# Optimization experiments

Hardware: AMD Instinct MI355X
Metric: run time of the kernel (lower is better)

Reference implementation:

```python
import jax, jax.numpy as jnp
import numpy as np

S = 7          # side
B = 2          # boxes per cell
C = 20         # classes
L = S * S      # grid cells
NOOBJ = 0.5 * 1.0
OBJ   = 0.5 * 1.0
CLS   = 0.5 * 1.0
COORD = 0.5 * 5.0


def setup_inputs() -> dict:
    key = jax.random.key(0)
    k1, k2, k3 = jax.random.split(key, 3)
    n = 16384
    preds = jax.random.uniform(k1, (n, L * (C + 5 * B)), dtype=jnp.float32)
    labels = jax.random.uniform(k2, (n, L * (1 + C + 4)), dtype=jnp.float32)
    lab = labels.reshape(n, L, 1 + C + 4)
    obj_flag = (jax.random.uniform(k3, (n, L)) < 0.15).astype(jnp.float32)
    lab = lab.at[:, :, 0].set(obj_flag)
    labels = lab.reshape(n, -1)
    return {"preds": preds, "labels": labels}


def _iou(t, o):
    # t, o: [..., 4] boxes in (cx, cy, w, h); returns [...]
    left   = jnp.maximum(t[..., 0] - 0.5 * t[..., 2], o[..., 0] - 0.5 * o[..., 2])
    right  = jnp.minimum(t[..., 0] + 0.5 * t[..., 2], o[..., 0] + 0.5 * o[..., 2])
    top    = jnp.maximum(t[..., 1] - 0.5 * t[..., 3], o[..., 1] - 0.5 * o[..., 3])
    bottom = jnp.minimum(t[..., 1] + 0.5 * t[..., 3], o[..., 1] + 0.5 * o[..., 3])
    w = right - left
    h = bottom - top
    invalid = (w < 0) | (h < 0)
    inter = jnp.where(invalid, 0.0, w * h)
    union = t[..., 2] * t[..., 3] + o[..., 2] * o[..., 3] - inter
    return jnp.where(invalid, 0.0, inter / jnp.maximum(union, 1e-12))


def reference(preds, labels):
    n = preds.shape[0]
    pcls  = preds[:, : L * C].reshape(n, L, C)                       # [n,L,C]
    pconf = preds[:, L * C : L * C + L * B].reshape(n, L, B)          # [n,L,B]
    pbox  = preds[:, L * C + L * B :].reshape(n, L, B, 4)             # [n,L,B,4]

    lab  = labels.reshape(n, L, 1 + C + 4)
    obj  = lab[:, :, 0] != 0                                          # [n,L]
    tcls = lab[:, :, 1 : 1 + C]                                       # [n,L,C]
    tbox = lab[:, :, 1 + C :]                                         # [n,L,4] raw

    # --- best-box selection (on detached predictions, like .detach() in torch) ---
    o_raw = jax.lax.stop_gradient(pbox)
    o = jnp.concatenate([o_raw[..., :2] / S, o_raw[..., 2:] ** 2], axis=-1)      # [n,L,B,4]
    t = jnp.concatenate([tbox[..., :2] / S, tbox[..., 2:]], axis=-1)[:, :, None] # [n,L,1,4]
    t = jax.lax.stop_gradient(t)

    iou  = _iou(t, o)                                                 # [n,L,B]
    rmse = jnp.sqrt(jnp.sum((t - o) ** 2, axis=-1))                   # [n,L,B]
    max_iou = jnp.max(iou, axis=-1)
    # if any IoU>0 pick first argmax of IoU, else first argmin of RMSE (best_rmse init 20)
    best = jnp.where(max_iou > 0, jnp.argmax(iou, axis=-1), jnp.argmin(rmse, axis=-1))  # [n,L]
    best_iou = jnp.take_along_axis(iou, best[:, :, None], axis=-1)[..., 0]        # [n,L]

    onehot = jnp.arange(B) == best[:, :, None]                        # [n,L,B]
    mask_best = obj[:, :, None] & onehot

    # confidence delta: noobject everywhere, overwritten at best box of object cells
    conf_delta = jnp.where(mask_best,
                           OBJ * (best_iou[:, :, None] - pconf) ** 2,
                           NOOBJ * pconf ** 2)

    # class delta (object cells only)
    cls_delta = jnp.where(obj[:, :, None], CLS * (tcls - pcls) ** 2, 0.0)

    # coord delta at best box: raw truth x,y and sqrt(truth w,h) vs raw preds
    pbest = jnp.take_along_axis(pbox, best[:, :, None, None], axis=2)[:, :, 0]    # [n,L,4]
    ttarget = jnp.concatenate([tbox[..., :2], jnp.sqrt(tbox[..., 2:])], axis=-1)  # [n,L,4]
    coord_delta = jnp.where(obj[:, :, None], COORD * (ttarget - pbest) ** 2, 0.0)

    return jnp.nansum(conf_delta) + jnp.nansum(cls_delta) + jnp.nansum(coord_delta)
```

## Files before the change

kernel.cpp:

```cpp
#include <hip/hip_runtime.h>


#define L_CELLS 49
#define PRED_ROW 1470
#define LAB_ROW 1225
#define CONF_BASE 980
#define BOX_BASE 1078
#define W_NOOBJ 0.5f
#define W_OBJ 0.5f
#define W_CLS 0.5f
#define W_COORD 2.5f
#define INV_S (1.0f / 7.0f)

__global__ __launch_bounds__(256) void yolo_loss_kernel(
    const float* __restrict__ preds, const float* __restrict__ labels,
    float* __restrict__ ws, int n) {
  int cell = blockIdx.x * blockDim.x + threadIdx.x;
  int total = n * L_CELLS;
  float acc = 0.0f;
  if (cell < total) {
    int sample = cell / L_CELLS;
    int l = cell - sample * L_CELLS;
    const float* rp = preds + (size_t)sample * PRED_ROW;
    const float* labc = labels + (size_t)sample * LAB_ROW + l * 25;

    float objf = labc[0];
    const float2 cf = *(const float2*)(rp + CONF_BASE + 2 * l);
    float c0 = cf.x, c1 = cf.y;

    if (objf != 0.0f) {
      const float* boxp = rp + BOX_BASE + 8 * l;
      float bx[8];
#pragma unroll
      for (int k = 0; k < 4; ++k) {
        float2 v = *(const float2*)(boxp + 2 * k);
        bx[2 * k] = v.x;
        bx[2 * k + 1] = v.y;
      }

      float tx = labc[21], ty = labc[22], tw = labc[23], th = labc[24];
      float t0 = tx * INV_S, t1 = ty * INV_S, t2 = tw, t3 = th;

      float iou[2], rmse2[2];
#pragma unroll
      for (int b = 0; b < 2; ++b) {
        float o0 = bx[4 * b + 0] * INV_S;
        float o1 = bx[4 * b + 1] * INV_S;
        float o2 = bx[4 * b + 2] * bx[4 * b + 2];
        float o3 = bx[4 * b + 3] * bx[4 * b + 3];
        float left = fmaxf(t0 - 0.5f * t2, o0 - 0.5f * o2);
        float right = fminf(t0 + 0.5f * t2, o0 + 0.5f * o2);
        float top = fmaxf(t1 - 0.5f * t3, o1 - 0.5f * o3);
        float bot = fminf(t1 + 0.5f * t3, o1 + 0.5f * o3);
        float w = right - left;
        float h = bot - top;
        bool invalid = (w < 0.0f) || (h < 0.0f);
        float inter = invalid ? 0.0f : w * h;
        float uni = t2 * t3 + o2 * o3 - inter;
        iou[b] = invalid ? 0.0f : inter / fmaxf(uni, 1e-12f);
        float d0 = t0 - o0, d1 = t1 - o1, d2 = t2 - o2, d3 = t3 - o3;
        rmse2[b] = d0 * d0 + d1 * d1 + d2 * d2 + d3 * d3;
      }

      float max_iou = fmaxf(iou[0], iou[1]);
      int best;
      if (max_iou > 0.0f)
        best = (iou[1] > iou[0]) ? 1 : 0;
      else
        best = (rmse2[1] < rmse2[0]) ? 1 : 0;
      float best_iou = iou[best];

      float cb = (best == 0) ? c0 : c1;
      float co = (best == 0) ? c1 : c0;
      float db = best_iou - cb;
      acc += W_OBJ * db * db + W_NOOBJ * co * co;

      const float* pcls = rp + l * 20;
      float clsacc = 0.0f;
#pragma unroll
      for (int c = 0; c < 20; ++c) {
        float d = labc[1 + c] - pcls[c];
        clsacc += d * d;
      }
      acc += W_CLS * clsacc;

      float e0 = tx - bx[best * 4 + 0];
      float e1 = ty - bx[best * 4 + 1];
      float e2 = sqrtf(tw) - bx[best * 4 + 2];
      float e3 = sqrtf(th) - bx[best * 4 + 3];
      acc += W_COORD * (e0 * e0 + e1 * e1 + e2 * e2 + e3 * e3);
    } else {
      acc = W_NOOBJ * (c0 * c0 + c1 * c1);
    }
  }

#pragma unroll
  for (int off = 32; off > 0; off >>= 1) acc += __shfl_down(acc, off);

  __shared__ float wsum[4];
  int wave = threadIdx.x >> 6;
  int lane = threadIdx.x & 63;
  if (lane == 0) wsum[wave] = acc;
  __syncthreads();
  if (threadIdx.x == 0) {
    ws[blockIdx.x] = wsum[0] + wsum[1] + wsum[2] + wsum[3];
  }
}

__global__ __launch_bounds__(256) void final_reduce_kernel(
    const float* __restrict__ ws, float* __restrict__ out, int m) {
  float acc = 0.0f;
  for (int i = threadIdx.x; i < m; i += 256) acc += ws[i];
#pragma unroll
  for (int off = 32; off > 0; off >>= 1) acc += __shfl_down(acc, off);
  __shared__ float wsum[4];
  int wave = threadIdx.x >> 6;
  int lane = threadIdx.x & 63;
  if (lane == 0) wsum[wave] = acc;
  __syncthreads();
  if (threadIdx.x == 0) out[0] = wsum[0] + wsum[1] + wsum[2] + wsum[3];
}

extern "C" void kernel_launch(void* const* d_in, const int* in_sizes, int n_in,
                              void* d_out, int out_size, void* d_ws, size_t ws_size,
                              hipStream_t stream) {
  const float* preds = (const float*)d_in[0];
  const float* labels = (const float*)d_in[1];
  float* out = (float*)d_out;
  float* ws = (float*)d_ws;
  int n = in_sizes[0] / PRED_ROW;
  int total = n * L_CELLS;
  int blocks = (total + 255) / 256;

  yolo_loss_kernel<<<blocks, 256, 0, stream>>>(preds, labels, ws, n);
  final_reduce_kernel<<<1, 256, 0, stream>>>(ws, out, blocks);
}
```

Baseline: 189.1 us.

## Stage per-sample rows in LDS with coalesced float4 loads, block per two samples

Each block now handles two samples. It copies their full prediction and label rows into shared memory with aligned float4 loads, then computes the class loss spread across all threads, one (cell, class) element each, while 49 threads handle the box and confidence logic. This replaces strided, uncoalesced per-cell global reads with contiguous vector loads. In exchange it reads every row in full even though only about 15% of cells need class data, and it adds LDS traffic, a block barrier and many idle threads during the box phase. The block count assumes n is divisible by two.

```diff
diff --git a/kernel.cpp b/kernel.cpp
--- a/kernel.cpp
+++ b/kernel.cpp
@@ -11,86 +11,113 @@
 #define W_CLS 0.5f
 #define W_COORD 2.5f
 #define INV_S (1.0f / 7.0f)
+#define SPB 2
 
 __global__ __launch_bounds__(256) void yolo_loss_kernel(
     const float* __restrict__ preds, const float* __restrict__ labels,
     float* __restrict__ ws, int n) {
-  int cell = blockIdx.x * blockDim.x + threadIdx.x;
-  int total = n * L_CELLS;
+  __shared__ float4 lab4[SPB][308];
+  __shared__ float4 pred4[SPB][368];
+
+  const int tid = threadIdx.x;
+  const int s0 = blockIdx.x * SPB;
+
+  const size_t ltotal = (size_t)n * LAB_ROW;
+  const size_t ptotal = (size_t)n * PRED_ROW;
+
+  int loff[SPB], poff[SPB];
+#pragma unroll
+  for (int r = 0; r < SPB; ++r) {
+    size_t lrow = (size_t)(s0 + r) * LAB_ROW;
+    size_t lstart = lrow & ~(size_t)3;
+    loff[r] = (int)(lrow - lstart);
+    for (int i = tid; i < 308; i += 256) {
+      size_t g = lstart + 4 * (size_t)i;
+      if (g > ltotal - 4) g = ltotal - 4;
+      lab4[r][i] = *(const float4*)(labels + g);
+    }
+    size_t prow = (size_t)(s0 + r) * PRED_ROW;
+    size_t pstart = prow & ~(size_t)3;
+    poff[r] = (int)(prow - pstart);
+    for (int i = tid; i < 368; i += 256) {
+      size_t g = pstart + 4 * (size_t)i;
+      if (g > ptotal - 4) g = ptotal - 4;
+      pred4[r][i] = *(const float4*)(preds + g);
+    }
+  }
+  __syncthreads();
+
   float acc = 0.0f;
-  if (cell < total) {
-    int sample = cell / L_CELLS;
-    int l = cell - sample * L_CELLS;
-    const float* rp = preds + (size_t)sample * PRED_ROW;
-    const float* labc = labels + (size_t)sample * LAB_ROW + l * 25;
 
-    float objf = labc[0];
-    const float2 cf = *(const float2*)(rp + CONF_BASE + 2 * l);
-    float c0 = cf.x, c1 = cf.y;
+#pragma unroll
+  for (int r = 0; r < SPB; ++r) {
+    const float* lab = (const float*)lab4[r] + loff[r];
+    const float* pr = (const float*)pred4[r] + poff[r];
 
-    if (objf != 0.0f) {
-      const float* boxp = rp + BOX_BASE + 8 * l;
-      float bx[8];
+    for (int idx = tid; idx < CONF_BASE; idx += 256) {
+      int l = idx / 20;
+      int c = idx - l * 20;
+      if (lab[l * 25] != 0.0f) {
+        float d = lab[l * 25 + 1 + c] - pr[idx];
+        acc += W_CLS * d * d;
+      }
+    }
+
+    if (tid < L_CELLS) {
+      int l = tid;
+      float objf = lab[l * 25];
+      float c0 = pr[CONF_BASE + 2 * l];
+      float c1 = pr[CONF_BASE + 2 * l + 1];
+      if (objf != 0.0f) {
+        float bx[8];
 #pragma unroll
-      for (int k = 0; k < 4; ++k) {
-        float2 v = *(const float2*)(boxp + 2 * k);
-        bx[2 * k] = v.x;
-        bx[2 * k + 1] = v.y;
+        for (int k = 0; k < 8; ++k) bx[k] = pr[BOX_BASE + 8 * l + k];
+        float tx = lab[l * 25 + 21], ty = lab[l * 25 + 22];
+        float tw = lab[l * 25 + 23], th = lab[l * 25 + 24];
+        float t0 = tx * INV_S, t1 = ty * INV_S, t2 = tw, t3 = th;
+
+        float iou[2], rmse2[2];
+#pragma unroll
+        for (int b = 0; b < 2; ++b) {
+          float o0 = bx[4 * b + 0] * INV_S;
+          float o1 = bx[4 * b + 1] * INV_S;
+          float o2 = bx[4 * b + 2] * bx[4 * b + 2];
+          float o3 = bx[4 * b + 3] * bx[4 * b + 3];
+          float left = fmaxf(t0 - 0.5f * t2, o0 - 0.5f * o2);
+          float right = fminf(t0 + 0.5f * t2, o0 + 0.5f * o2);
+          float top = fmaxf(t1 - 0.5f * t3, o1 - 0.5f * o3);
+          float bot = fminf(t1 + 0.5f * t3, o1 + 0.5f * o3);
+          float w = right - left;
+          float h = bot - top;
+          bool invalid = (w < 0.0f) || (h < 0.0f);
+          float inter = invalid ? 0.0f : w * h;
+          float uni = t2 * t3 + o2 * o3 - inter;
+          iou[b] = invalid ? 0.0f : inter / fmaxf(uni, 1e-12f);
+          float d0 = t0 - o0, d1 = t1 - o1, d2 = t2 - o2, d3 = t3 - o3;
+          rmse2[b] = d0 * d0 + d1 * d1 + d2 * d2 + d3 * d3;
+        }
+
+        float max_iou = fmaxf(iou[0], iou[1]);
+        int best;
+        if (max_iou > 0.0f)
+          best = (iou[1] > iou[0]) ? 1 : 0;
+        else
+          best = (rmse2[1] < rmse2[0]) ? 1 : 0;
+        float best_iou = iou[best];
+
+        float cb = (best == 0) ? c0 : c1;
+        float co = (best == 0) ? c1 : c0;
+        float db = best_iou - cb;
+        acc += W_OBJ * db * db + W_NOOBJ * co * co;
+
+        float e0 = tx - bx[best * 4 + 0];
+        float e1 = ty - bx[best * 4 + 1];
+        float e2 = sqrtf(tw) - bx[best * 4 + 2];
+        float e3 = sqrtf(th) - bx[best * 4 + 3];
+        acc += W_COORD * (e0 * e0 + e1 * e1 + e2 * e2 + e3 * e3);
+      } else {
+        acc += W_NOOBJ * (c0 * c0 + c1 * c1);
       }
-
-      float tx = labc[21], ty = labc[22], tw = labc[23], th = labc[24];
-      float t0 = tx * INV_S, t1 = ty * INV_S, t2 = tw, t3 = th;
-
-      float iou[2], rmse2[2];
-#pragma unroll
-      for (int b = 0; b < 2; ++b) {
-        float o0 = bx[4 * b + 0] * INV_S;
-        float o1 = bx[4 * b + 1] * INV_S;
-        float o2 = bx[4 * b + 2] * bx[4 * b + 2];
-        float o3 = bx[4 * b + 3] * bx[4 * b + 3];
-        float left = fmaxf(t0 - 0.5f * t2, o0 - 0.5f * o2);
-        float right = fminf(t0 + 0.5f * t2, o0 + 0.5f * o2);
-        float top = fmaxf(t1 - 0.5f * t3, o1 - 0.5f * o3);
-        float bot = fminf(t1 + 0.5f * t3, o1 + 0.5f * o3);
-        float w = right - left;
-        float h = bot - top;
-        bool invalid = (w < 0.0f) || (h < 0.0f);
-        float inter = invalid ? 0.0f : w * h;
-        float uni = t2 * t3 + o2 * o3 - inter;
-        iou[b] = invalid ? 0.0f : inter / fmaxf(uni, 1e-12f);
-        float d0 = t0 - o0, d1 = t1 - o1, d2 = t2 - o2, d3 = t3 - o3;
-        rmse2[b] = d0 * d0 + d1 * d1 + d2 * d2 + d3 * d3;
-      }
-
-      float max_iou = fmaxf(iou[0], iou[1]);
-      int best;
-      if (max_iou > 0.0f)
-        best = (iou[1] > iou[0]) ? 1 : 0;
-      else
-        best = (rmse2[1] < rmse2[0]) ? 1 : 0;
-      float best_iou = iou[best];
-
-      float cb = (best == 0) ? c0 : c1;
-      float co = (best == 0) ? c1 : c0;
-      float db = best_iou - cb;
-      acc += W_OBJ * db * db + W_NOOBJ * co * co;
-
-      const float* pcls = rp + l * 20;
-      float clsacc = 0.0f;
-#pragma unroll
-      for (int c = 0; c < 20; ++c) {
-        float d = labc[1 + c] - pcls[c];
-        clsacc += d * d;
-      }
-      acc += W_CLS * clsacc;
-
-      float e0 = tx - bx[best * 4 + 0];
-      float e1 = ty - bx[best * 4 + 1];
-      float e2 = sqrtf(tw) - bx[best * 4 + 2];
-      float e3 = sqrtf(th) - bx[best * 4 + 3];
-      acc += W_COORD * (e0 * e0 + e1 * e1 + e2 * e2 + e3 * e3);
-    } else {
-      acc = W_NOOBJ * (c0 * c0 + c1 * c1);
     }
   }
 
@@ -98,13 +125,11 @@
   for (int off = 32; off > 0; off >>= 1) acc += __shfl_down(acc, off);
 
   __shared__ float wsum[4];
-  int wave = threadIdx.x >> 6;
-  int lane = threadIdx.x & 63;
+  int wave = tid >> 6;
+  int lane = tid & 63;
   if (lane == 0) wsum[wave] = acc;
   __syncthreads();
-  if (threadIdx.x == 0) {
-    ws[blockIdx.x] = wsum[0] + wsum[1] + wsum[2] + wsum[3];
-  }
+  if (tid == 0) ws[blockIdx.x] = wsum[0] + wsum[1] + wsum[2] + wsum[3];
 }
 
 __global__ __launch_bounds__(256) void final_reduce_kernel(
@@ -129,8 +154,7 @@
   float* out = (float*)d_out;
   float* ws = (float*)d_ws;
   int n = in_sizes[0] / PRED_ROW;
-  int total = n * L_CELLS;
-  int blocks = (total + 255) / 256;
+  int blocks = n / SPB;
 
   yolo_loss_kernel<<<blocks, 256, 0, stream>>>(preds, labels, ws, n);
   final_reduce_kernel<<<1, 256, 0, stream>>>(ws, out, blocks);
```

Result: slower. 211.3 us (+11.8%).

## Map one wavefront per sample and stage label rows in LDS via float4 loads

Applied to the files above, without the earlier changes.

Each block now handles four samples, one per 64-lane wavefront, with lanes 0-48 mapping to grid cells. The whole label row is first copied into shared memory with coalesced float4 loads, replacing the strided 25-float-per-thread global reads. Class predictions are read as float2. The goal is to cut uncoalesced label traffic. In exchange 15 of 64 lanes sit idle, the kernel assumes n is a multiple of 4, and no barrier separates the LDS writes from the reads, which only works because each wave reads just its own slot.

```diff
diff --git a/kernel.cpp b/kernel.cpp
--- a/kernel.cpp
+++ b/kernel.cpp
@@ -14,31 +14,41 @@
 
 __global__ __launch_bounds__(256) void yolo_loss_kernel(
     const float* __restrict__ preds, const float* __restrict__ labels,
-    float* __restrict__ ws, int n) {
-  int cell = blockIdx.x * blockDim.x + threadIdx.x;
-  int total = n * L_CELLS;
+    float* __restrict__ ws) {
+  __shared__ float4 labs4[4][312];
+
+  const int tid = threadIdx.x;
+  const int w = tid >> 6;
+  const int lane = tid & 63;
+  const int s = blockIdx.x * 4 + w;
+
+  size_t g0 = (size_t)s * LAB_ROW;
+  size_t a = g0 & ~(size_t)3;
+  int off = (int)(g0 - a);
+  for (int i = lane; i < 307; i += 64) {
+    labs4[w][i] = *(const float4*)(labels + a + 4 * (size_t)i);
+  }
+
+  const float* lab = (const float*)labs4[w] + off;
+  const float* rp = preds + (size_t)s * PRED_ROW;
+
   float acc = 0.0f;
-  if (cell < total) {
-    int sample = cell / L_CELLS;
-    int l = cell - sample * L_CELLS;
-    const float* rp = preds + (size_t)sample * PRED_ROW;
-    const float* labc = labels + (size_t)sample * LAB_ROW + l * 25;
-
-    float objf = labc[0];
-    const float2 cf = *(const float2*)(rp + CONF_BASE + 2 * l);
+  if (lane < L_CELLS) {
+    const int l = lane;
+    float2 cf = *(const float2*)(rp + CONF_BASE + 2 * l);
     float c0 = cf.x, c1 = cf.y;
+    float objf = lab[25 * l];
 
     if (objf != 0.0f) {
-      const float* boxp = rp + BOX_BASE + 8 * l;
       float bx[8];
 #pragma unroll
       for (int k = 0; k < 4; ++k) {
-        float2 v = *(const float2*)(boxp + 2 * k);
+        float2 v = *(const float2*)(rp + BOX_BASE + 8 * l + 2 * k);
         bx[2 * k] = v.x;
         bx[2 * k + 1] = v.y;
       }
-
-      float tx = labc[21], ty = labc[22], tw = labc[23], th = labc[24];
+      float tx = lab[25 * l + 21], ty = lab[25 * l + 22];
+      float tw = lab[25 * l + 23], th = lab[25 * l + 24];
       float t0 = tx * INV_S, t1 = ty * INV_S, t2 = tw, t3 = th;
 
       float iou[2], rmse2[2];
@@ -52,10 +62,10 @@
         float right = fminf(t0 + 0.5f * t2, o0 + 0.5f * o2);
         float top = fmaxf(t1 - 0.5f * t3, o1 - 0.5f * o3);
         float bot = fminf(t1 + 0.5f * t3, o1 + 0.5f * o3);
-        float w = right - left;
+        float wd = right - left;
         float h = bot - top;
-        bool invalid = (w < 0.0f) || (h < 0.0f);
-        float inter = invalid ? 0.0f : w * h;
+        bool invalid = (wd < 0.0f) || (h < 0.0f);
+        float inter = invalid ? 0.0f : wd * h;
         float uni = t2 * t3 + o2 * o3 - inter;
         iou[b] = invalid ? 0.0f : inter / fmaxf(uni, 1e-12f);
         float d0 = t0 - o0, d1 = t1 - o1, d2 = t2 - o2, d3 = t3 - o3;
@@ -75,12 +85,13 @@
       float db = best_iou - cb;
       acc += W_OBJ * db * db + W_NOOBJ * co * co;
 
-      const float* pcls = rp + l * 20;
       float clsacc = 0.0f;
 #pragma unroll
-      for (int c = 0; c < 20; ++c) {
-        float d = labc[1 + c] - pcls[c];
-        clsacc += d * d;
+      for (int k = 0; k < 10; ++k) {
+        float2 p = *(const float2*)(rp + 20 * l + 2 * k);
+        float d0 = lab[25 * l + 1 + 2 * k] - p.x;
+        float d1 = lab[25 * l + 2 + 2 * k] - p.y;
+        clsacc += d0 * d0 + d1 * d1;
       }
       acc += W_CLS * clsacc;
 
@@ -90,21 +101,17 @@
       float e3 = sqrtf(th) - bx[best * 4 + 3];
       acc += W_COORD * (e0 * e0 + e1 * e1 + e2 * e2 + e3 * e3);
     } else {
-      acc = W_NOOBJ * (c0 * c0 + c1 * c1);
+      acc += W_NOOBJ * (c0 * c0 + c1 * c1);
     }
   }
 
 #pragma unroll
-  for (int off = 32; off > 0; off >>= 1) acc += __shfl_down(acc, off);
+  for (int o = 32; o > 0; o >>= 1) acc += __shfl_down(acc, o);
 
   __shared__ float wsum[4];
-  int wave = threadIdx.x >> 6;
-  int lane = threadIdx.x & 63;
-  if (lane == 0) wsum[wave] = acc;
+  if (lane == 0) wsum[w] = acc;
   __syncthreads();
-  if (threadIdx.x == 0) {
-    ws[blockIdx.x] = wsum[0] + wsum[1] + wsum[2] + wsum[3];
-  }
+  if (tid == 0) ws[blockIdx.x] = wsum[0] + wsum[1] + wsum[2] + wsum[3];
 }
 
 __global__ __launch_bounds__(256) void final_reduce_kernel(
@@ -112,7 +119,7 @@
   float acc = 0.0f;
   for (int i = threadIdx.x; i < m; i += 256) acc += ws[i];
 #pragma unroll
-  for (int off = 32; off > 0; off >>= 1) acc += __shfl_down(acc, off);
+  for (int o = 32; o > 0; o >>= 1) acc += __shfl_down(acc, o);
   __shared__ float wsum[4];
   int wave = threadIdx.x >> 6;
   int lane = threadIdx.x & 63;
@@ -129,9 +136,8 @@
   float* out = (float*)d_out;
   float* ws = (float*)d_ws;
   int n = in_sizes[0] / PRED_ROW;
-  int total = n * L_CELLS;
-  int blocks = (total + 255) / 256;
+  int blocks = n / 4;
 
-  yolo_loss_kernel<<<blocks, 256, 0, stream>>>(preds, labels, ws, n);
+  yolo_loss_kernel<<<blocks, 256, 0, stream>>>(preds, labels, ws);
   final_reduce_kernel<<<1, 256, 0, stream>>>(ws, out, blocks);
 }
```

Result: no change. 189.1 us (-0.0%).
